# Kernel optimization log

Measured on AMD Instinct MI355X. Metric: run time of the kernel, lower is better.

## Reference

```python
import jax, jax.numpy as jnp
import numpy as np

B, T, F, H = 128, 256, 64, 512


def _lstm_cell(x, h, c, Wih, Whh, bih, bhh):
    # PyTorch gate order: i, f, g, o
    g = x @ Wih.T + h @ Whh.T + bih + bhh  # [B, 4H]
    i, f, gg, o = jnp.split(g, 4, axis=-1)
    i = jax.nn.sigmoid(i)
    f = jax.nn.sigmoid(f)
    gg = jnp.tanh(gg)
    o = jax.nn.sigmoid(o)
    c = f * c + i * gg
    h = o * jnp.tanh(c)
    return h, c


def setup_inputs() -> dict:
    key = jax.random.key(0)
    ks = jax.random.split(key, 20)
    s = lambda k, shp: (jax.random.normal(k, shp, jnp.float32) * 0.05)
    return {
        "x": jax.random.normal(ks[0], (B, T, F), jnp.float32),
        # encoder LSTM (2 layers)
        "enc_Wih0": s(ks[1], (4 * H, F)), "enc_Whh0": s(ks[2], (4 * H, H)),
        "enc_bih0": s(ks[3], (4 * H,)), "enc_bhh0": s(ks[4], (4 * H,)),
        "enc_Wih1": s(ks[5], (4 * H, H)), "enc_Whh1": s(ks[6], (4 * H, H)),
        "enc_bih1": s(ks[7], (4 * H,)), "enc_bhh1": s(ks[8], (4 * H,)),
        # decoder LSTM (2 layers)
        "dec_Wih0": s(ks[9], (4 * H, F)), "dec_Whh0": s(ks[10], (4 * H, H)),
        "dec_bih0": s(ks[11], (4 * H,)), "dec_bhh0": s(ks[12], (4 * H,)),
        "dec_Wih1": s(ks[13], (4 * H, H)), "dec_Whh1": s(ks[14], (4 * H, H)),
        "dec_bih1": s(ks[15], (4 * H,)), "dec_bhh1": s(ks[16], (4 * H,)),
        # decoder output projection
        "lin_W": s(ks[17], (F, H)), "lin_b": s(ks[18], (F,)),
    }


def reference(x, enc_Wih0, enc_Whh0, enc_bih0, enc_bhh0,
              enc_Wih1, enc_Whh1, enc_bih1, enc_bhh1,
              dec_Wih0, dec_Whh0, dec_bih0, dec_bhh0,
              dec_Wih1, dec_Whh1, dec_bih1, dec_bhh1,
              lin_W, lin_b):
    b, t, f = x.shape
    zeros = jnp.zeros((b, H), x.dtype)

    # ---- encoder: stacked 2-layer LSTM over time, keep only final (h, c) ----
    def enc_step(carry, xt):
        h0, c0, h1, c1 = carry
        h0, c0 = _lstm_cell(xt, h0, c0, enc_Wih0, enc_Whh0, enc_bih0, enc_bhh0)
        h1, c1 = _lstm_cell(h0, h1, c1, enc_Wih1, enc_Whh1, enc_bih1, enc_bhh1)
        return (h0, c0, h1, c1), None

    (h0, c0, h1, c1), _ = jax.lax.scan(enc_step, (zeros, zeros, zeros, zeros),
                                       jnp.swapaxes(x, 0, 1))  # [T, B, F]

    def dec_step(carry, _):
        xin, h0, c0, h1, c1 = carry
        h0, c0 = _lstm_cell(xin, h0, c0, dec_Wih0, dec_Whh0, dec_bih0, dec_bhh0)
        h1, c1 = _lstm_cell(h0, h1, c1, dec_Wih1, dec_Whh1, dec_bih1, dec_bhh1)
        out = h1 @ lin_W.T + lin_b  # [B, F]
        return (out, h0, c0, h1, c1), out

    x_last = x[:, -1, :]
    _, ys = jax.lax.scan(dec_step, (x_last, h0, c0, h1, c1), None, length=t)
    # generated step j fills output index t-1-j -> reverse time axis
    return jnp.flip(jnp.swapaxes(ys, 0, 1), axis=1)  # [B, T, F]
```

## Files before the change

kernel.cpp:

```cpp
#include <hip/hip_runtime.h>
#include <math.h>

#define T_ 256
#define H_ 512
#define NWG 256
#define NTHR 256
#define WPG 64

typedef _Float16 half8 __attribute__((ext_vector_type(8)));
typedef float f32x4 __attribute__((ext_vector_type(4)));
typedef unsigned short u16;
typedef unsigned int u32;
typedef unsigned long long u64;

#define O_H0R  0u
#define O_H1R  2097152u
#define O_BAR  4194304u

#define E0W 0u
#define E1W 36864u
#define D0W 0u
#define D1W 65536u

__device__ __forceinline__ float sigf(float x) { return 1.0f / (1.0f + expf(-x)); }

__device__ __forceinline__ u16 f2h_bits(float f) {
    _Float16 h = (_Float16)f;
    return __builtin_bit_cast(u16, h);
}
__device__ __forceinline__ float h2f(u16 x) {
    return (float)__builtin_bit_cast(_Float16, x);
}

__device__ __forceinline__ void llc_store64(u64* p, u64 v) {
    __hip_atomic_store(p, v, __ATOMIC_RELAXED, __HIP_MEMORY_SCOPE_AGENT);
}
__device__ __forceinline__ void llc_store32(u32* p, u32 v) {
    __hip_atomic_store(p, v, __ATOMIC_RELAXED, __HIP_MEMORY_SCOPE_AGENT);
}

__device__ __forceinline__ void gbar_arrive(int* flags, int w, int gen) {
    asm volatile("s_waitcnt vmcnt(0)" ::: "memory");
    __syncthreads();
    if (threadIdx.x == 0)
        __hip_atomic_store(flags + w * 16, gen, __ATOMIC_RELAXED, __HIP_MEMORY_SCOPE_AGENT);
}
__device__ __forceinline__ void gbar_wait(int* flags, int gbase, int gen, bool inv) {
    if (threadIdx.x < 64) {
        while (__hip_atomic_load(flags + (gbase + threadIdx.x) * 16,
                                 __ATOMIC_RELAXED, __HIP_MEMORY_SCOPE_AGENT) < gen)
            __builtin_amdgcn_s_sleep(1);
    }
    __syncthreads();
    if (inv) {
        if (threadIdx.x == 0) __builtin_amdgcn_fence(__ATOMIC_ACQUIRE, "agent");
        __syncthreads();
    }
}

__device__ __forceinline__ void st_w(char* smem, unsigned base, unsigned K2,
                                     unsigned m, unsigned k, float v) {
    _Float16 hh = (_Float16)v;
    unsigned off = (m * K2 + k * 2) ^ ((m & 7) << 4);
    *(u16*)(smem + base + off) = __builtin_bit_cast(u16, hh);
}

__device__ __forceinline__ void load_plane(uint4 (&buf)[16], const u32* __restrict__ plane,
                                           unsigned loff) {
    #pragma unroll
    for (int i = 0; i < 16; ++i)
        buf[i] = *(const uint4*)(plane + (size_t)i * 2048 + loff);
}

__device__ __forceinline__ void cons_plane(const uint4 (&buf)[16], const char* __restrict__ smem,
                                           unsigned base, unsigned K2, unsigned wk0,
                                           unsigned R, unsigned qq, f32x4& acc) {
    const unsigned swz = (R & 7) << 4;
    #pragma unroll
    for (int i = 0; i < 16; ++i) {
        const unsigned wb = R * K2 + (wk0 + (unsigned)i * 32 + qq * 8) * 2;
        half8 av = *(const half8*)(smem + base + (wb ^ swz));
        half8 bv = __builtin_bit_cast(half8, buf[i]);
        acc = __builtin_amdgcn_mfma_f32_16x16x32_f16(av, bv, acc, 0, 0, 0);
    }
}

__device__ __forceinline__ void seg_x(
    const char* smem, unsigned base, unsigned K2,
    const float* __restrict__ x, int t, unsigned bt, unsigned R, int lane, f32x4& acc) {
    const unsigned mm = lane & 15, qq = lane >> 4;
    const unsigned swz = (R & 7) << 4;
    const float* xp = x + ((size_t)(bt + mm) * T_ + t) * 64 + qq * 8;
    #pragma unroll
    for (int i = 0; i < 2; ++i) {
        float4 f0 = *(const float4*)(xp + i * 32);
        float4 f1 = *(const float4*)(xp + i * 32 + 4);
        float fs[8] = { f0.x, f0.y, f0.z, f0.w, f1.x, f1.y, f1.z, f1.w };
        half8 bv;
        #pragma unroll
        for (int j = 0; j < 8; ++j) bv[j] = (_Float16)fs[j];
        unsigned wb = (R * K2 + (qq * 8 + i * 32) * 2) ^ swz;
        half8 av = *(const half8*)(smem + base + wb);
        acc = __builtin_amdgcn_mfma_f32_16x16x32_f16(av, bv, acc, 0, 0, 0);
    }
}

__device__ __forceinline__ void epilogue_reg(f32x4 acc, const float* bz, int u, int b,
                                             float& cr, u32* hw, int lane) {
    float gi = sigf(acc[0] + bz[0]);
    float gf = sigf(acc[1] + bz[1]);
    float gt = tanhf(acc[2] + bz[2]);
    float go = sigf(acc[3] + bz[3]);
    float cn = gf * cr + gi * gt;
    cr = cn;
    float hv = go * tanhf(cn);
    u16 mybits = f2h_bits(hv);
    int other = __shfl_xor((int)(u32)mybits, 16);
    if (((lane >> 4) & 1) == 0) {
        u32 pk = (u32)mybits | (((u32)other & 0xFFFFu) << 16);
        unsigned idx = (unsigned)(u >> 5) * 2048 + (unsigned)b * 16 + ((unsigned)(u & 31) >> 1);
        llc_store32(hw + idx, pk);
    }
}

__device__ __forceinline__ void linear_out(const u32* __restrict__ h1p,
                                           const float* __restrict__ linW,
                                           const float* __restrict__ linb,
                                           float* __restrict__ out, int g, int wl,
                                           int tid, int t) {
    const int bl = g * 32 + (wl >> 1);
    const int kq = tid & 7;
    const int f  = (wl & 1) * 32 + (tid >> 3);
    float s = 0.f;
    #pragma unroll
    for (int c2 = 0; c2 < 2; ++c2) {
        const int ch = kq * 2 + c2;
        const u64* ph = (const u64*)h1p + (size_t)ch * 1024 + (size_t)bl * 8;
        const float* wp = linW + (size_t)f * H_ + ch * 32;
        #pragma unroll
        for (int j = 0; j < 8; ++j) {
            u64 r = ph[j];
            s += h2f((u16)r)         * wp[4 * j + 0];
            s += h2f((u16)(r >> 16)) * wp[4 * j + 1];
            s += h2f((u16)(r >> 32)) * wp[4 * j + 2];
            s += h2f((u16)(r >> 48)) * wp[4 * j + 3];
        }
    }
    s += __shfl_xor(s, 1);
    s += __shfl_xor(s, 2);
    s += __shfl_xor(s, 4);
    if (kq == 0)
        out[((size_t)bl * T_ + (255 - t)) * 64 + f] = s + linb[f];
}

__global__ __launch_bounds__(NTHR, 1) void lstm_persist(
    const float* __restrict__ x,
    const float* __restrict__ eWih0, const float* __restrict__ eWhh0,
    const float* __restrict__ ebih0, const float* __restrict__ ebhh0,
    const float* __restrict__ eWih1, const float* __restrict__ eWhh1,
    const float* __restrict__ ebih1, const float* __restrict__ ebhh1,
    const float* __restrict__ dWih0, const float* __restrict__ dWhh0,
    const float* __restrict__ dbih0, const float* __restrict__ dbhh0,
    const float* __restrict__ dWih1, const float* __restrict__ dWhh1,
    const float* __restrict__ dbih1, const float* __restrict__ dbhh1,
    const float* __restrict__ linW,  const float* __restrict__ linb,
    float* __restrict__ out, char* __restrict__ wsb, int* __restrict__ flags) {
    extern __shared__ char smem[];
    const int w = blockIdx.x, tid = threadIdx.x;
    const int lane = tid & 63, wave = tid >> 6;

    const int g = w >> 6;
    const int wl = w & 63;
    const int gbase = g * WPG;
    const int u_base = wl * 8;
    const int mh = wave >> 1;
    const int bh = wave & 1;
    const int u = u_base + mh * 4 + (lane >> 4);
    const unsigned bt = (unsigned)(g * 32 + bh * 16);
    const int b = (int)bt + (lane & 15);
    const unsigned R = (unsigned)(mh * 16 + (lane & 15));
    const unsigned qq = (unsigned)(lane >> 4);
    const unsigned loff = (bt + (unsigned)(lane & 15)) * 16 + qq * 4;

    #define H0S(t) ((u32*)(wsb + O_H0R + (unsigned)((t) & 15) * 131072u))
    #define H1S(t) ((u32*)(wsb + O_H1R + (unsigned)((t) & 15) * 131072u))
    int gen = 0;

    {
        const int gtid = wl * NTHR + tid;
        if (gtid < 12288) {
            const int slot  = gtid >> 12;
            const int rem   = gtid & 4095;
            const int chunk = rem >> 8;
            const int brow  = (rem & 255) >> 3;
            const int q     = rem & 7;
            u64* base = (slot == 0) ? (u64*)(wsb + O_H0R + 15u * 131072u)
                      : (slot == 1) ? (u64*)(wsb + O_H1R + 14u * 131072u)
                                    : (u64*)(wsb + O_H1R + 15u * 131072u);
            llc_store64(base + (size_t)chunk * 1024 + (size_t)(g * 32 + brow) * 8 + q, 0ULL);
        }
    }
    float bzA[4], bzB[4], bzD0[4], bzD0b[4], bzD1[4];
    #pragma unroll
    for (int gg = 0; gg < 4; ++gg) {
        const int gr = gg * H_ + u;
        bzA[gg] = ebih0[gr] + ebhh0[gr];
        bzB[gg] = ebih1[gr] + ebhh1[gr];
        float d0 = dbih0[gr] + dbhh0[gr];
        bzD0[gg] = d0;
        float s = 0.f;
        for (int f = 0; f < 64; ++f) s += dWih0[(size_t)gr * 64 + f] * linb[f];
        bzD0b[gg] = d0 + s;
        bzD1[gg] = dbih1[gr] + dbhh1[gr];
    }
    float c0r = 0.f, c1r = 0.f;

    for (int mr = 0; mr < 32; ++mr) {
        const int gr = (mr & 3) * H_ + u_base + (mr >> 2);
        for (int k = tid; k < 576; k += NTHR) {
            float v = (k < 64) ? eWih0[(size_t)gr * 64 + k] : eWhh0[(size_t)gr * H_ + (k - 64)];
            st_w(smem, E0W, 1152, mr, k, v);
        }
        for (int k = tid; k < 1024; k += NTHR) {
            float v = (k < 512) ? eWih1[(size_t)gr * H_ + k] : eWhh1[(size_t)gr * H_ + (k - 512)];
            st_w(smem, E1W, 2048, mr, k, v);
        }
    }
    gbar_arrive(flags, w, ++gen);
    gbar_wait(flags, gbase, gen, false);

    uint4 P[16], Q[16];

    for (int p = 0; p <= T_; ++p) {
        gbar_arrive(flags, w, ++gen);
        f32x4 a = {0,0,0,0}, e = {0,0,0,0};
        if (p < T_) seg_x(smem, E0W, 1152, x, p, bt, R, lane, a);
        gbar_wait(flags, gbase, gen, p > 0 && (p & 15) == 0);
        load_plane(P, H0S(p - 1), loff);
        if (p >= 1) load_plane(Q, H1S(p - 2), loff);
        if (p < T_) cons_plane(P, smem, E0W, 1152, 64, R, qq, a);
        if (p >= 1) {
            cons_plane(P, smem, E1W, 2048, 0,   R, qq, e);
            cons_plane(Q, smem, E1W, 2048, 512, R, qq, e);
        }
        if (p < T_)  epilogue_reg(a, bzA, u, b, c0r, H0S(p), lane);
        if (p >= 1)  epilogue_reg(e, bzB, u, b, c1r, H1S(p - 1), lane);
    }

    __syncthreads();
    for (int mr = 0; mr < 32; ++mr) {
        const int gr = (mr & 3) * H_ + u_base + (mr >> 2);
        const float* wr = dWih0 + (size_t)gr * 64;
        for (int c = tid; c < 512; c += NTHR) {
            float s = 0.f;
            #pragma unroll 8
            for (int f = 0; f < 64; ++f) s += wr[f] * linW[(size_t)f * H_ + c];
            st_w(smem, D0W, 2048, mr, c, s);
            st_w(smem, D0W, 2048, mr, 512 + c, dWhh0[(size_t)gr * H_ + c]);
            st_w(smem, D1W, 2048, mr, c,       dWih1[(size_t)gr * H_ + c]);
            st_w(smem, D1W, 2048, mr, 512 + c, dWhh1[(size_t)gr * H_ + c]);
        }
    }
    __syncthreads();

    for (int t = 0; t < T_; ++t) {
        {
            gbar_arrive(flags, w, ++gen);
            f32x4 a = {0,0,0,0};
            if (t > 0) {
                cons_plane(Q, smem, D0W, 2048, 512, R, qq, a);
            } else {
                const float* xr = x + ((size_t)b * T_ + (T_ - 1)) * 64;
                #pragma unroll
                for (int gg = 0; gg < 4; ++gg) {
                    const float* wr = dWih0 + (size_t)(gg * H_ + u) * 64;
                    float s = 0.f;
                    for (int f = 0; f < 64; ++f) s += wr[f] * xr[f];
                    a[gg] = s;
                }
            }
            gbar_wait(flags, gbase, gen, t > 0 && (t & 15) == 0);
            if (t > 0) {
                load_plane(P, H1S(t - 1), loff);
                cons_plane(P, smem, D0W, 2048, 0, R, qq, a);
            } else {
                load_plane(Q, H0S(-1), loff);
                cons_plane(Q, smem, D0W, 2048, 512, R, qq, a);
            }
            epilogue_reg(a, (t > 0) ? bzD0b : bzD0, u, b, c0r, H0S(t), lane);
        }
        {
            gbar_arrive(flags, w, ++gen);
            f32x4 e = {0,0,0,0};
            if (t > 0) {
                cons_plane(P, smem, D1W, 2048, 512, R, qq, e);
                linear_out(H1S(t - 1), linW, linb, out, g, wl, tid, t - 1);
            }
            gbar_wait(flags, gbase, gen, false);
            load_plane(Q, H0S(t), loff);
            if (t == 0) {
                load_plane(P, H1S(-1), loff);
                cons_plane(P, smem, D1W, 2048, 512, R, qq, e);
            }
            cons_plane(Q, smem, D1W, 2048, 0, R, qq, e);
            epilogue_reg(e, bzD1, u, b, c1r, H1S(t), lane);
        }
    }
    gbar_arrive(flags, w, ++gen);
    gbar_wait(flags, gbase, gen, false);
    linear_out(H1S(255), linW, linb, out, g, wl, tid, 255);
}

extern "C" void kernel_launch(void* const* d_in, const int* in_sizes, int n_in,
                              void* d_out, int out_size, void* d_ws, size_t ws_size,
                              hipStream_t stream) {
    (void)in_sizes; (void)n_in; (void)out_size; (void)ws_size;
    const float* x     = (const float*)d_in[0];
    const float* eWih0 = (const float*)d_in[1];
    const float* eWhh0 = (const float*)d_in[2];
    const float* ebih0 = (const float*)d_in[3];
    const float* ebhh0 = (const float*)d_in[4];
    const float* eWih1 = (const float*)d_in[5];
    const float* eWhh1 = (const float*)d_in[6];
    const float* ebih1 = (const float*)d_in[7];
    const float* ebhh1 = (const float*)d_in[8];
    const float* dWih0 = (const float*)d_in[9];
    const float* dWhh0 = (const float*)d_in[10];
    const float* dbih0 = (const float*)d_in[11];
    const float* dbhh0 = (const float*)d_in[12];
    const float* dWih1 = (const float*)d_in[13];
    const float* dWhh1 = (const float*)d_in[14];
    const float* dbih1 = (const float*)d_in[15];
    const float* dbhh1 = (const float*)d_in[16];
    const float* linW  = (const float*)d_in[17];
    const float* linb  = (const float*)d_in[18];

    char* wsb  = (char*)d_ws;
    int* flags = (int*)(wsb + O_BAR);

    static const int lds_bytes = 131072;
    hipFuncSetAttribute((const void*)lstm_persist,
                        hipFuncAttributeMaxDynamicSharedMemorySize, lds_bytes);

    hipMemsetAsync(flags, 0, NWG * 64, stream);

    hipLaunchKernelGGL(lstm_persist, dim3(NWG), dim3(NTHR), lds_bytes, stream,
                       x, eWih0, eWhh0, ebih0, ebhh0, eWih1, eWhh1, ebih1, ebhh1,
                       dWih0, dWhh0, dbih0, dbhh0, dWih1, dWhh1, dbih1, dbhh1,
                       linW, linb, (float*)d_out, wsb, flags);
}
```

Measured before the change: 3.731 ms.

## Replace full group barrier with per-chunk readiness waits overlapping loads and MFMA

Replaces the all-64-workgroup barrier wait before each recurrent matmul with a fine-grained wait: wave 0 polls the group's flags, builds a bitmask of which 4-workgroup chunks have published their hidden-state slice, and shares it through an LDS word. Each 32-wide K chunk is then loaded and consumed as soon as its producers are ready, so loads and MFMAs start before the slowest workgroup arrives. Steps that need a cache-invalidate fence keep the old full barrier. This adds repeated ballot/poll overhead and an LDS word, and risks spin contention or subtle ordering issues since relaxed atomics are used without an acquire per chunk.

Measured after the change: 5.181 ms. 1.39x slower.

```diff
diff --git a/kernel.cpp b/kernel.cpp
--- a/kernel.cpp
+++ b/kernel.cpp
@@ -21,6 +21,7 @@
 #define E1W 36864u
 #define D0W 0u
 #define D1W 65536u
+#define RDYW 131072u
 
 __device__ __forceinline__ float sigf(float x) { return 1.0f / (1.0f + expf(-x)); }
 
@@ -58,6 +59,39 @@
     }
 }
 
+__device__ __forceinline__ void chunk_wait(int* flags, int gbase, int gen,
+                                           u32* rdyw, int wave, int lane, int c,
+                                           unsigned& cached) {
+    if (!(cached & (1u << c))) {
+        if (wave == 0) {
+            for (;;) {
+                int fl = __hip_atomic_load(flags + (gbase + lane) * 16,
+                                           __ATOMIC_RELAXED, __HIP_MEMORY_SCOPE_AGENT);
+                u64 bal = __ballot(fl >= gen);
+                unsigned m = 0;
+                #pragma unroll
+                for (int cc = 0; cc < 16; ++cc)
+                    if (((bal >> (4 * cc)) & 0xFULL) == 0xFULL) m |= (1u << cc);
+                if (lane == 0)
+                    __hip_atomic_store(rdyw, ((unsigned)gen << 16) | m,
+                                       __ATOMIC_RELAXED, __HIP_MEMORY_SCOPE_WORKGROUP);
+                cached = m;
+                if (cached & (1u << c)) break;
+                __builtin_amdgcn_s_sleep(1);
+            }
+        } else {
+            for (;;) {
+                u32 wv = __hip_atomic_load(rdyw, __ATOMIC_RELAXED,
+                                           __HIP_MEMORY_SCOPE_WORKGROUP);
+                cached = ((wv >> 16) == ((unsigned)gen & 0xFFFFu)) ? (wv & 0xFFFFu) : 0u;
+                if (cached & (1u << c)) break;
+                __builtin_amdgcn_s_sleep(1);
+            }
+        }
+    }
+    __builtin_amdgcn_sched_barrier(0);
+}
+
 __device__ __forceinline__ void st_w(char* smem, unsigned base, unsigned K2,
                                      unsigned m, unsigned k, float v) {
     _Float16 hh = (_Float16)v;
@@ -65,6 +99,10 @@
     *(u16*)(smem + base + off) = __builtin_bit_cast(u16, hh);
 }
 
+__device__ __forceinline__ uint4 ld_chunk(const u32* __restrict__ plane, int c, unsigned loff) {
+    return *(const uint4*)(plane + (size_t)c * 2048 + loff);
+}
+
 __device__ __forceinline__ void load_plane(uint4 (&buf)[16], const u32* __restrict__ plane,
                                            unsigned loff) {
     #pragma unroll
@@ -72,17 +110,22 @@
         buf[i] = *(const uint4*)(plane + (size_t)i * 2048 + loff);
 }
 
+__device__ __forceinline__ void cons_chunk(uint4 bv4, const char* __restrict__ smem,
+                                           unsigned base, unsigned K2, unsigned wk0,
+                                           int c, unsigned R, unsigned qq, f32x4& acc) {
+    const unsigned swz = (R & 7) << 4;
+    const unsigned wb = R * K2 + (wk0 + (unsigned)c * 32 + qq * 8) * 2;
+    half8 av = *(const half8*)(smem + base + (wb ^ swz));
+    half8 bv = __builtin_bit_cast(half8, bv4);
+    acc = __builtin_amdgcn_mfma_f32_16x16x32_f16(av, bv, acc, 0, 0, 0);
+}
+
 __device__ __forceinline__ void cons_plane(const uint4 (&buf)[16], const char* __restrict__ smem,
                                            unsigned base, unsigned K2, unsigned wk0,
                                            unsigned R, unsigned qq, f32x4& acc) {
-    const unsigned swz = (R & 7) << 4;
     #pragma unroll
-    for (int i = 0; i < 16; ++i) {
-        const unsigned wb = R * K2 + (wk0 + (unsigned)i * 32 + qq * 8) * 2;
-        half8 av = *(const half8*)(smem + base + (wb ^ swz));
-        half8 bv = __builtin_bit_cast(half8, buf[i]);
-        acc = __builtin_amdgcn_mfma_f32_16x16x32_f16(av, bv, acc, 0, 0, 0);
-    }
+    for (int i = 0; i < 16; ++i)
+        cons_chunk(buf[i], smem, base, K2, wk0, i, R, qq, acc);
 }
 
 __device__ __forceinline__ void seg_x(
@@ -181,6 +224,7 @@
     const unsigned R = (unsigned)(mh * 16 + (lane & 15));
     const unsigned qq = (unsigned)(lane >> 4);
     const unsigned loff = (bt + (unsigned)(lane & 15)) * 16 + qq * 4;
+    u32* rdyw = (u32*)(smem + RDYW);
 
     #define H0S(t) ((u32*)(wsb + O_H0R + (unsigned)((t) & 15) * 131072u))
     #define H1S(t) ((u32*)(wsb + O_H1R + (unsigned)((t) & 15) * 131072u))
@@ -235,13 +279,40 @@
         gbar_arrive(flags, w, ++gen);
         f32x4 a = {0,0,0,0}, e = {0,0,0,0};
         if (p < T_) seg_x(smem, E0W, 1152, x, p, bt, R, lane, a);
-        gbar_wait(flags, gbase, gen, p > 0 && (p & 15) == 0);
-        load_plane(P, H0S(p - 1), loff);
-        if (p >= 1) load_plane(Q, H1S(p - 2), loff);
-        if (p < T_) cons_plane(P, smem, E0W, 1152, 64, R, qq, a);
-        if (p >= 1) {
+        const bool fence = (p > 0 && (p & 15) == 0);
+        if (fence) {
+            gbar_wait(flags, gbase, gen, true);
+            load_plane(P, H0S(p - 1), loff);
+            load_plane(Q, H1S(p - 2), loff);
+            if (p < T_) cons_plane(P, smem, E0W, 1152, 64, R, qq, a);
             cons_plane(P, smem, E1W, 2048, 0,   R, qq, e);
             cons_plane(Q, smem, E1W, 2048, 512, R, qq, e);
+        } else {
+            const u32* pp = H0S(p - 1);
+            const u32* qp = H1S(p - 2);
+            unsigned cached = 0;
+            uint4 pl, ql = {0, 0, 0, 0};
+            chunk_wait(flags, gbase, gen, rdyw, wave, lane, 0, cached);
+            pl = ld_chunk(pp, 0, loff);
+            if (p >= 1) ql = ld_chunk(qp, 0, loff);
+            #pragma unroll
+            for (int c = 1; c < 16; ++c) {
+                chunk_wait(flags, gbase, gen, rdyw, wave, lane, c, cached);
+                uint4 pn = ld_chunk(pp, c, loff);
+                uint4 qn = {0, 0, 0, 0};
+                if (p >= 1) qn = ld_chunk(qp, c, loff);
+                if (p < T_) cons_chunk(pl, smem, E0W, 1152, 64, c - 1, R, qq, a);
+                if (p >= 1) {
+                    cons_chunk(pl, smem, E1W, 2048, 0,   c - 1, R, qq, e);
+                    cons_chunk(ql, smem, E1W, 2048, 512, c - 1, R, qq, e);
+                }
+                pl = pn; ql = qn;
+            }
+            if (p < T_) cons_chunk(pl, smem, E0W, 1152, 64, 15, R, qq, a);
+            if (p >= 1) {
+                cons_chunk(pl, smem, E1W, 2048, 0,   15, R, qq, e);
+                cons_chunk(ql, smem, E1W, 2048, 512, 15, R, qq, e);
+            }
         }
         if (p < T_)  epilogue_reg(a, bzA, u, b, c0r, H0S(p), lane);
         if (p >= 1)  epilogue_reg(e, bzB, u, b, c1r, H1S(p - 1), lane);
@@ -267,6 +338,7 @@
         {
             gbar_arrive(flags, w, ++gen);
             f32x4 a = {0,0,0,0};
+            const bool fence = (t > 0 && (t & 15) == 0);
             if (t > 0) {
                 cons_plane(Q, smem, D0W, 2048, 512, R, qq, a);
             } else {
@@ -279,13 +351,27 @@
                     a[gg] = s;
                 }
             }
-            gbar_wait(flags, gbase, gen, t > 0 && (t & 15) == 0);
-            if (t > 0) {
-                load_plane(P, H1S(t - 1), loff);
-                cons_plane(P, smem, D0W, 2048, 0, R, qq, a);
+            if (t == 0 || fence) {
+                gbar_wait(flags, gbase, gen, fence);
+                if (t > 0) {
+                    load_plane(P, H1S(t - 1), loff);
+                    cons_plane(P, smem, D0W, 2048, 0, R, qq, a);
+                } else {
+                    load_plane(Q, H0S(-1), loff);
+                    cons_plane(Q, smem, D0W, 2048, 512, R, qq, a);
+                }
             } else {
-                load_plane(Q, H0S(-1), loff);
-                cons_plane(Q, smem, D0W, 2048, 512, R, qq, a);
+                const u32* pp = H1S(t - 1);
+                unsigned cached = 0;
+                chunk_wait(flags, gbase, gen, rdyw, wave, lane, 0, cached);
+                P[0] = ld_chunk(pp, 0, loff);
+                #pragma unroll
+                for (int c = 1; c < 16; ++c) {
+                    chunk_wait(flags, gbase, gen, rdyw, wave, lane, c, cached);
+                    P[c] = ld_chunk(pp, c, loff);
+                    cons_chunk(P[c - 1], smem, D0W, 2048, 0, c - 1, R, qq, a);
+                }
+                cons_chunk(P[15], smem, D0W, 2048, 0, 15, R, qq, a);
             }
             epilogue_reg(a, (t > 0) ? bzD0b : bzD0, u, b, c0r, H0S(t), lane);
         }
@@ -296,13 +382,25 @@
                 cons_plane(P, smem, D1W, 2048, 512, R, qq, e);
                 linear_out(H1S(t - 1), linW, linb, out, g, wl, tid, t - 1);
             }
-            gbar_wait(flags, gbase, gen, false);
-            load_plane(Q, H0S(t), loff);
             if (t == 0) {
+                gbar_wait(flags, gbase, gen, false);
+                load_plane(Q, H0S(0), loff);
                 load_plane(P, H1S(-1), loff);
                 cons_plane(P, smem, D1W, 2048, 512, R, qq, e);
-            }
-            cons_plane(Q, smem, D1W, 2048, 0, R, qq, e);
+                cons_plane(Q, smem, D1W, 2048, 0,   R, qq, e);
+            } else {
+                const u32* qp = H0S(t);
+                unsigned cached = 0;
+                chunk_wait(flags, gbase, gen, rdyw, wave, lane, 0, cached);
+                Q[0] = ld_chunk(qp, 0, loff);
+                #pragma unroll
+                for (int c = 1; c < 16; ++c) {
+                    chunk_wait(flags, gbase, gen, rdyw, wave, lane, c, cached);
+                    Q[c] = ld_chunk(qp, c, loff);
+                    cons_chunk(Q[c - 1], smem, D1W, 2048, 0, c - 1, R, qq, e);
+                }
+                cons_chunk(Q[15], smem, D1W, 2048, 0, 15, R, qq, e);
+            }
             epilogue_reg(e, bzD1, u, b, c1r, H1S(t), lane);
         }
     }
@@ -338,7 +436,7 @@
     char* wsb  = (char*)d_ws;
     int* flags = (int*)(wsb + O_BAR);
 
-    static const int lds_bytes = 131072;
+    static const int lds_bytes = 131072 + 16;
     hipFuncSetAttribute((const void*)lstm_persist,
                         hipFuncAttributeMaxDynamicSharedMemorySize, lds_bytes);
 
```
